# Kernel tuning notes

Hardware: AMD Instinct MI355X
Metric: run time of the kernel (lower is better)

## Reference

```python
import jax, jax.numpy as jnp
import numpy as np

B, T, D, H = 8, 2048, 2048, 128  # batch, seq_len, d_model, head_size
NEG = -1e9


def setup_inputs() -> dict:
    key = jax.random.key(0)
    k0, k1, k2, k3 = jax.random.split(key, 4)
    x = jax.random.normal(k0, (B, T, D), dtype=jnp.float32)
    s = 1.0 / np.sqrt(D)
    Wq = jax.random.normal(k1, (D, H), dtype=jnp.float32) * s
    Wk = jax.random.normal(k2, (D, H), dtype=jnp.float32) * s
    Wv = jax.random.normal(k3, (D, H), dtype=jnp.float32) * s
    return {"x": x, "Wq": Wq, "Wk": Wk, "Wv": Wv}


def reference(x, Wq, Wk, Wv):
    # projections: [B,T,H]
    q = jnp.einsum('btd,dh->bth', x, Wq)
    k = jnp.einsum('btd,dh->bth', x, Wk)
    v = jnp.einsum('btd,dh->bth', x, Wv)
    # NOTE: module multiplies by sqrt(head_size) (faithful to source)
    wei = jnp.einsum('bqh,bkh->bqk', q, k) * jnp.sqrt(jnp.float32(H))
    causal = jnp.tril(jnp.ones((T, T), dtype=bool))
    wei = jnp.where(causal, wei, jnp.float32(NEG))
    wei = jax.nn.softmax(wei, axis=-1)
    # dropout is identity (deterministic=True / rate=0)
    out = jnp.einsum('bqk,bkh->bqh', wei, v)
    return out
```

## Files before the change

kernel.cpp:

```cpp
#include <hip/hip_runtime.h>
#include <math.h>

#define B_ 8
#define T_ 2048
#define D_ 2048
#define H_ 128
#define M_ (B_ * T_)

typedef __bf16 bf16x8 __attribute__((ext_vector_type(8)));
typedef __bf16 bf16x4 __attribute__((ext_vector_type(4)));
typedef float f32x4 __attribute__((ext_vector_type(4)));

#define MFMA(a, b, c) __builtin_amdgcn_mfma_f32_16x16x32_bf16(a, b, c, 0, 0, 0)

#define QH_OFF 0
#define QL_OFF (1 * 2097152)
#define KH_OFF (2 * 2097152)
#define KL_OFF (3 * 2097152)
#define VT_OFF (4 * 2097152)
#define WTH_OFF (5 * 2097152)
#define WTL_OFF (WTH_OFF + 786432)

__global__ __launch_bounds__(256) void prep_kernel(
    const float* __restrict__ Wq, const float* __restrict__ Wk,
    const float* __restrict__ Wv, __bf16* __restrict__ wpk_hi,
    __bf16* __restrict__ wpk_lo) {
  const int z = blockIdx.y;
  const int k0 = blockIdx.x * 64;
  const float* W = z == 0 ? Wq : z == 1 ? Wk : Wv;
  __shared__ float tile[64][132];
  const int t = threadIdx.x;
#pragma unroll
  for (int it = 0; it < 8; ++it) {
    int f4 = it * 256 + t;
    int row = f4 >> 5, c = (f4 & 31) << 2;
    *(float4*)&tile[row][c] = *(const float4*)&W[(size_t)(k0 + row) * H_ + c];
  }
  __syncthreads();
  int n = t >> 1, kh = (t & 1) << 5;
  __bf16 h[32], l[32];
#pragma unroll
  for (int kk = 0; kk < 32; ++kk) {
    float x = tile[kh + kk][n];
    __bf16 hi = (__bf16)x;
    h[kk] = hi;
    l[kk] = (__bf16)(x - (float)hi);
  }
  const int nf = z * H_ + n;
  const int g = nf >> 4, l15 = nf & 15;
  const int s = (k0 + kh) >> 5;
#pragma unroll
  for (int c = 0; c < 4; ++c) {
    size_t dst = ((size_t)(g * 64 + s) * 64 + c * 16 + l15) * 8;
    *(bf16x8*)&wpk_hi[dst] = *(bf16x8*)&h[c * 8];
    *(bf16x8*)&wpk_lo[dst] = *(bf16x8*)&l[c * 8];
  }
}

#define XSTR 72

#define PROJ_STEP(KS, CH, CL, NH, NL)                                      \
  {                                                                        \
    __syncthreads();                                                       \
    {                                                                      \
      __bf16 h0 = (__bf16)xr.x, h1 = (__bf16)xr.y, h2 = (__bf16)xr.z,      \
             h3 = (__bf16)xr.w;                                            \
      bf16x4 hv = {h0, h1, h2, h3};                                        \
      bf16x4 lv = {(__bf16)(xr.x - (float)h0), (__bf16)(xr.y - (float)h1), \
                   (__bf16)(xr.z - (float)h2), (__bf16)(xr.w - (float)h3)};\
      *(bf16x4*)&Xs[xm * XSTR + xk] = hv;                                  \
      *(bf16x4*)&Xs[xm * XSTR + 32 + xk] = lv;                             \
    }                                                                      \
    if ((KS) < 63) {                                                       \
      const int ko = ((KS) + 1) << 5;                                      \
      xr = *(const float4*)(xgp + ko);                                     \
      _Pragma("unroll") for (int nt = 0; nt < 3; ++nt) {                   \
        NH[nt] = *(const bf16x8*)(wph[nt] + ((KS) + 1) * 512);             \
        NL[nt] = *(const bf16x8*)(wpl[nt] + ((KS) + 1) * 512);             \
      }                                                                    \
    }                                                                      \
    __syncthreads();                                                       \
    bf16x8 ah[2], al[2];                                                   \
    _Pragma("unroll") for (int mg = 0; mg < 2; ++mg) {                     \
      ah[mg] = *(bf16x8*)&Xs[(wr * 32 + mg * 16 + l15) * XSTR + q8];       \
      al[mg] = *(bf16x8*)&Xs[(wr * 32 + mg * 16 + l15) * XSTR + 32 + q8];  \
    }                                                                      \
    _Pragma("unroll") for (int nt = 0; nt < 3; ++nt) {                     \
      _Pragma("unroll") for (int mg = 0; mg < 2; ++mg) {                   \
        acc[mg][nt] = MFMA(ah[mg], CH[nt], acc[mg][nt]);                   \
        acc[mg][nt] = MFMA(al[mg], CH[nt], acc[mg][nt]);                   \
        acc[mg][nt] = MFMA(ah[mg], CL[nt], acc[mg][nt]);                   \
      }                                                                    \
    }                                                                      \
  }

__global__ __launch_bounds__(512, 4) void proj_kernel(
    const float* __restrict__ X, const __bf16* __restrict__ wpk_hi,
    const __bf16* __restrict__ wpk_lo, __bf16* __restrict__ qh,
    __bf16* __restrict__ ql, __bf16* __restrict__ kh,
    __bf16* __restrict__ kl, __bf16* __restrict__ vt) {
  __shared__ __align__(16) __bf16 Xs[64 * XSTR];
  const int t = threadIdx.x;
  const int wv = t >> 6, lane = t & 63;
  const int l15 = lane & 15, quad = lane >> 4, q8 = quad * 8;
  const int bi = blockIdx.x;
  const int m0 = (bi >> 1) * 64;
  const int nbase = (bi & 1) * 192;
  const int wr = wv >> 2, wc = wv & 3;
  const int xm = t >> 3, xk = (t & 7) << 2;
  const float* xgp = X + (size_t)(m0 + xm) * D_ + xk;
  const __bf16* wph[3];
  const __bf16* wpl[3];
#pragma unroll
  for (int nt = 0; nt < 3; ++nt) {
    int g = (nbase >> 4) + wc * 3 + nt;
    size_t off = (size_t)g * 32768 + (size_t)lane * 8;
    wph[nt] = wpk_hi + off;
    wpl[nt] = wpk_lo + off;
  }
  f32x4 acc[2][3] = {};
  float4 xr = *(const float4*)xgp;
  bf16x8 wha[3], wla[3], whb[3], wlb[3];
#pragma unroll
  for (int nt = 0; nt < 3; ++nt) {
    wha[nt] = *(const bf16x8*)(wph[nt]);
    wla[nt] = *(const bf16x8*)(wpl[nt]);
  }
  for (int ks2 = 0; ks2 < 64; ks2 += 2) {
    PROJ_STEP(ks2, wha, wla, whb, wlb);
    PROJ_STEP(ks2 + 1, whb, wlb, wha, wla);
  }
#pragma unroll
  for (int nt = 0; nt < 3; ++nt) {
    int ncb = nbase + wc * 48 + nt * 16;
    int z = ncb >> 7;
    int h = (ncb & 127) + l15;
#pragma unroll
    for (int mg = 0; mg < 2; ++mg) {
      int r0 = m0 + wr * 32 + mg * 16 + quad * 4;
      if (z == 2) {
        int b = m0 >> 11;
        int tt0 = (m0 & 2047) + wr * 32 + mg * 16 + quad * 4;
        bf16x4 pv = {(__bf16)acc[mg][nt][0], (__bf16)acc[mg][nt][1],
                     (__bf16)acc[mg][nt][2], (__bf16)acc[mg][nt][3]};
        *(bf16x4*)&vt[(size_t)(b * H_ + h) * T_ + tt0] = pv;
      } else {
        __bf16* dh = z == 0 ? qh : kh;
        __bf16* dl = z == 0 ? ql : kl;
#pragma unroll
        for (int reg = 0; reg < 4; ++reg) {
          float v = acc[mg][nt][reg];
          __bf16 hi = (__bf16)v;
          dh[(size_t)(r0 + reg) * H_ + h] = hi;
          dl[(size_t)(r0 + reg) * H_ + h] = (__bf16)(v - (float)hi);
        }
      }
    }
  }
}

__global__ __launch_bounds__(512, 2) void attn_kernel(
    const __bf16* __restrict__ qh, const __bf16* __restrict__ qlo,
    const __bf16* __restrict__ kh, const __bf16* __restrict__ klo,
    const __bf16* __restrict__ vt, float* __restrict__ out) {
  const int t = threadIdx.x;
  const int wv = t >> 6, st = wv >> 2, cw = wv & 3;
  const int lane = t & 63, l15 = lane & 15, quad = lane >> 4;
  const int j = blockIdx.x, b = j & 7, pi = j >> 3;
  const int qlidx = (st == 0) ? pi : 63 - pi;
  const int t0 = qlidx * 32;
  const int nkt = (qlidx >> 1) + 1;
  __shared__ __align__(16) __bf16 Pbuf[8][32 * 72];
  __shared__ __align__(16) float Obuf[2][32 * 132];
  __shared__ float mlb[2][4][32], llb[2][4][32];
  const size_t qrow0 = (size_t)b * T_ + t0;
  bf16x8 qfh[2][4], qfl[2][4];
#pragma unroll
  for (int mg = 0; mg < 2; ++mg)
#pragma unroll
    for (int ds = 0; ds < 4; ++ds) {
      size_t off = (qrow0 + mg * 16 + l15) * H_ + ds * 32 + quad * 8;
      qfh[mg][ds] = *(const bf16x8*)(qh + off);
      qfl[mg][ds] = *(const bf16x8*)(qlo + off);
    }
  f32x4 O[2][8] = {};
  float ms[2][4], ls[2][4];
#pragma unroll
  for (int mg = 0; mg < 2; ++mg)
#pragma unroll
    for (int reg = 0; reg < 4; ++reg) {
      ms[mg][reg] = -INFINITY;
      ls[mg][reg] = 0.f;
    }
  const __bf16* vtb = vt + (size_t)b * H_ * T_;
  const float scale = 11.313708498984761f;
  for (int kt_i = cw; kt_i < nkt; kt_i += 4) {
    const int kt = kt_i * 64;
    f32x4 S[2][4] = {};
#pragma unroll
    for (int ds = 0; ds < 4; ++ds)
#pragma unroll
      for (int ct = 0; ct < 4; ++ct) {
        size_t koff =
            ((size_t)b * T_ + kt + ct * 16 + l15) * H_ + ds * 32 + quad * 8;
        bf16x8 bh = *(const bf16x8*)(kh + koff);
        bf16x8 bl = *(const bf16x8*)(klo + koff);
#pragma unroll
        for (int mg = 0; mg < 2; ++mg) {
          S[mg][ct] = MFMA(qfh[mg][ds], bh, S[mg][ct]);
          S[mg][ct] = MFMA(qfl[mg][ds], bh, S[mg][ct]);
          S[mg][ct] = MFMA(qfh[mg][ds], bl, S[mg][ct]);
        }
      }
    const bool diag = (kt_i == nkt - 1);
#pragma unroll
    for (int mg = 0; mg < 2; ++mg)
#pragma unroll
      for (int ct = 0; ct < 4; ++ct)
#pragma unroll
        for (int reg = 0; reg < 4; ++reg) {
          float s = S[mg][ct][reg] * scale;
          if (diag && (kt + ct * 16 + l15 > t0 + mg * 16 + quad * 4 + reg))
            s = -1e30f;
          S[mg][ct][reg] = s;
        }
    float al_[2][4];
#pragma unroll
    for (int mg = 0; mg < 2; ++mg)
#pragma unroll
      for (int reg = 0; reg < 4; ++reg) {
        float r = fmaxf(fmaxf(S[mg][0][reg], S[mg][1][reg]),
                        fmaxf(S[mg][2][reg], S[mg][3][reg]));
        r = fmaxf(r, __shfl_xor(r, 1));
        r = fmaxf(r, __shfl_xor(r, 2));
        r = fmaxf(r, __shfl_xor(r, 4));
        r = fmaxf(r, __shfl_xor(r, 8));
        float mn = fmaxf(ms[mg][reg], r);
        float a = __expf(ms[mg][reg] - mn);
        ms[mg][reg] = mn;
        float ps = 0.f;
#pragma unroll
        for (int ct = 0; ct < 4; ++ct) {
          float p = __expf(S[mg][ct][reg] - mn);
          S[mg][ct][reg] = p;
          ps += p;
        }
        ps += __shfl_xor(ps, 1);
        ps += __shfl_xor(ps, 2);
        ps += __shfl_xor(ps, 4);
        ps += __shfl_xor(ps, 8);
        ls[mg][reg] = ls[mg][reg] * a + ps;
        al_[mg][reg] = a;
      }
#pragma unroll
    for (int mg = 0; mg < 2; ++mg)
#pragma unroll
      for (int ht = 0; ht < 8; ++ht)
#pragma unroll
        for (int reg = 0; reg < 4; ++reg) O[mg][ht][reg] *= al_[mg][reg];
#pragma unroll
    for (int mg = 0; mg < 2; ++mg)
#pragma unroll
      for (int ct = 0; ct < 4; ++ct)
#pragma unroll
        for (int reg = 0; reg < 4; ++reg)
          Pbuf[wv][(mg * 16 + quad * 4 + reg) * 72 + ct * 16 + l15] =
              (__bf16)S[mg][ct][reg];
#pragma unroll
    for (int ks = 0; ks < 2; ++ks) {
      bf16x8 pf0 = *(bf16x8*)&Pbuf[wv][(l15)*72 + ks * 32 + quad * 8];
      bf16x8 pf1 = *(bf16x8*)&Pbuf[wv][(16 + l15) * 72 + ks * 32 + quad * 8];
#pragma unroll
      for (int ht = 0; ht < 8; ++ht) {
        bf16x8 vf = *(const bf16x8*)&vtb[(size_t)(ht * 16 + l15) * T_ + kt +
                                         ks * 32 + quad * 8];
        O[0][ht] = MFMA(pf0, vf, O[0][ht]);
        O[1][ht] = MFMA(pf1, vf, O[1][ht]);
      }
    }
  }
  if (l15 == 0) {
#pragma unroll
    for (int mg = 0; mg < 2; ++mg)
#pragma unroll
      for (int reg = 0; reg < 4; ++reg) {
        mlb[st][cw][mg * 16 + quad * 4 + reg] = ms[mg][reg];
        llb[st][cw][mg * 16 + quad * 4 + reg] = ls[mg][reg];
      }
  }
  for (int i = t; i < 2 * 32 * 132; i += 512) ((float*)Obuf)[i] = 0.f;
  __syncthreads();
  float aw[2][4];
#pragma unroll
  for (int mg = 0; mg < 2; ++mg)
#pragma unroll
    for (int reg = 0; reg < 4; ++reg) {
      int row = mg * 16 + quad * 4 + reg;
      float M = fmaxf(fmaxf(mlb[st][0][row], mlb[st][1][row]),
                      fmaxf(mlb[st][2][row], mlb[st][3][row]));
      float L = 0.f;
#pragma unroll
      for (int w = 0; w < 4; ++w)
        L += llb[st][w][row] * __expf(mlb[st][w][row] - M);
      aw[mg][reg] = __expf(ms[mg][reg] - M) / L;
    }
#pragma unroll
  for (int mg = 0; mg < 2; ++mg)
#pragma unroll
    for (int ht = 0; ht < 8; ++ht)
#pragma unroll
      for (int reg = 0; reg < 4; ++reg)
        atomicAdd(&Obuf[st][(mg * 16 + quad * 4 + reg) * 132 + ht * 16 + l15],
                  O[mg][ht][reg] * aw[mg][reg]);
  __syncthreads();
  {
    const int stw = t >> 8, tt = t & 255;
    const int qlw = (stw == 0) ? pi : 63 - pi;
    const size_t obase = ((size_t)b * T_ + qlw * 32) * H_;
#pragma unroll
    for (int i = 0; i < 4; ++i) {
      int f4 = i * 256 + tt;
      int row = f4 >> 5, c = (f4 & 31) << 2;
      *(float4*)&out[obase + (size_t)row * H_ + c] =
          *(float4*)&Obuf[stw][row * 132 + c];
    }
  }
}

extern "C" void kernel_launch(void* const* d_in, const int* in_sizes, int n_in,
                              void* d_out, int out_size, void* d_ws, size_t ws_size,
                              hipStream_t stream) {
  const float* x = (const float*)d_in[0];
  const float* Wq = (const float*)d_in[1];
  const float* Wk = (const float*)d_in[2];
  const float* Wv = (const float*)d_in[3];
  __bf16* ws = (__bf16*)d_ws;
  float* out = (float*)d_out;
  prep_kernel<<<dim3(32, 3), 256, 0, stream>>>(Wq, Wk, Wv, ws + WTH_OFF,
                                               ws + WTL_OFF);
  proj_kernel<<<512, 512, 0, stream>>>(x, ws + WTH_OFF, ws + WTL_OFF,
                                       ws + QH_OFF, ws + QL_OFF, ws + KH_OFF,
                                       ws + KL_OFF, ws + VT_OFF);
  attn_kernel<<<256, 512, 0, stream>>>(ws + QH_OFF, ws + QL_OFF, ws + KH_OFF,
                                       ws + KL_OFF, ws + VT_OFF, out);
}
```

Before: 397.8 us.

## Stage projection weights through LDS and prefetch two K-steps ahead

The prep kernel now writes the split hi/lo bf16 weights in a plain transposed [N][D] layout instead of an MFMA-fragment-packed layout. The projection kernel cooperatively loads each 32-wide K slice of the weights into LDS and reads MFMA B fragments from there, so each weight element is fetched from global memory once per block rather than once per wave row. Global prefetch now runs two K-steps ahead using double register sets. In exchange it adds about 28KB of LDS traffic and extra LDS reads per step, which may reduce occupancy or cause bank conflicts.

```diff
diff --git a/kernel.cpp b/kernel.cpp
--- a/kernel.cpp
+++ b/kernel.cpp
@@ -23,8 +23,8 @@
 
 __global__ __launch_bounds__(256) void prep_kernel(
     const float* __restrict__ Wq, const float* __restrict__ Wk,
-    const float* __restrict__ Wv, __bf16* __restrict__ wpk_hi,
-    __bf16* __restrict__ wpk_lo) {
+    const float* __restrict__ Wv, __bf16* __restrict__ wt_hi,
+    __bf16* __restrict__ wt_lo) {
   const int z = blockIdx.y;
   const int k0 = blockIdx.x * 64;
   const float* W = z == 0 ? Wq : z == 1 ? Wk : Wv;
@@ -46,59 +46,78 @@
     h[kk] = hi;
     l[kk] = (__bf16)(x - (float)hi);
   }
-  const int nf = z * H_ + n;
-  const int g = nf >> 4, l15 = nf & 15;
-  const int s = (k0 + kh) >> 5;
+  size_t base = (size_t)(z * H_ + n) * D_ + k0 + kh;
 #pragma unroll
   for (int c = 0; c < 4; ++c) {
-    size_t dst = ((size_t)(g * 64 + s) * 64 + c * 16 + l15) * 8;
-    *(bf16x8*)&wpk_hi[dst] = *(bf16x8*)&h[c * 8];
-    *(bf16x8*)&wpk_lo[dst] = *(bf16x8*)&l[c * 8];
+    *(bf16x8*)&wt_hi[base + c * 8] = *(bf16x8*)&h[c * 8];
+    *(bf16x8*)&wt_lo[base + c * 8] = *(bf16x8*)&l[c * 8];
   }
 }
 
+#define WSTR 36
 #define XSTR 72
 
-#define PROJ_STEP(KS, CH, CL, NH, NL)                                      \
+#define PSTEP(KS, XR, WRG)                                                 \
   {                                                                        \
-    __syncthreads();                                                       \
+    __syncthreads();                 \
     {                                                                      \
-      __bf16 h0 = (__bf16)xr.x, h1 = (__bf16)xr.y, h2 = (__bf16)xr.z,      \
-             h3 = (__bf16)xr.w;                                            \
+      __bf16 h0 = (__bf16)XR.x, h1 = (__bf16)XR.y, h2 = (__bf16)XR.z,      \
+             h3 = (__bf16)XR.w;                                            \
       bf16x4 hv = {h0, h1, h2, h3};                                        \
-      bf16x4 lv = {(__bf16)(xr.x - (float)h0), (__bf16)(xr.y - (float)h1), \
-                   (__bf16)(xr.z - (float)h2), (__bf16)(xr.w - (float)h3)};\
+      bf16x4 lv = {(__bf16)(XR.x - (float)h0), (__bf16)(XR.y - (float)h1), \
+                   (__bf16)(XR.z - (float)h2), (__bf16)(XR.w - (float)h3)};\
       *(bf16x4*)&Xs[xm * XSTR + xk] = hv;                                  \
       *(bf16x4*)&Xs[xm * XSTR + 32 + xk] = lv;                             \
     }                                                                      \
-    if ((KS) < 63) {                                                       \
-      const int ko = ((KS) + 1) << 5;                                      \
-      xr = *(const float4*)(xgp + ko);                                     \
-      _Pragma("unroll") for (int nt = 0; nt < 3; ++nt) {                   \
-        NH[nt] = *(const bf16x8*)(wph[nt] + ((KS) + 1) * 512);             \
-        NL[nt] = *(const bf16x8*)(wpl[nt] + ((KS) + 1) * 512);             \
+    _Pragma("unroll") for (int p = 0; p < 3; ++p) {                        \
+      bf16x4 a, b;                                                         \
+      _Pragma("unroll") for (int jj = 0; jj < 4; ++jj) {                   \
+        a[jj] = WRG[p][jj];                                                \
+        b[jj] = WRG[p][jj + 4];                                            \
       }                                                                    \
-    }                                                                      \
-    __syncthreads();                                                       \
+      *(bf16x4*)(wdst[p]) = a;                                             \
+      *(bf16x4*)(wdst[p] + 4) = b;                                         \
+    }                                                                      \
+    if ((KS) < 62) {     \
+      const int ko = ((KS) + 2) << 5;                                      \
+      XR = *(const float4*)(xgp + ko);                                     \
+      _Pragma("unroll") for (int p = 0; p < 3; ++p)                        \
+        WRG[p] = *(const bf16x8*)(wsrc[p] + ko);                           \
+    }                                                                      \
+    __syncthreads();                              \
     bf16x8 ah[2], al[2];                                                   \
     _Pragma("unroll") for (int mg = 0; mg < 2; ++mg) {                     \
       ah[mg] = *(bf16x8*)&Xs[(wr * 32 + mg * 16 + l15) * XSTR + q8];       \
       al[mg] = *(bf16x8*)&Xs[(wr * 32 + mg * 16 + l15) * XSTR + 32 + q8];  \
     }                                                                      \
     _Pragma("unroll") for (int nt = 0; nt < 3; ++nt) {                     \
+      const int n = wc * 48 + nt * 16 + l15;                               \
+      bf16x4 b0 = *(bf16x4*)&Wh[n * WSTR + q8];                            \
+      bf16x4 b1 = *(bf16x4*)&Wh[n * WSTR + q8 + 4];                        \
+      bf16x4 b2 = *(bf16x4*)&Wl[n * WSTR + q8];                            \
+      bf16x4 b3 = *(bf16x4*)&Wl[n * WSTR + q8 + 4];                        \
+      bf16x8 bh, bl;                                                       \
+      _Pragma("unroll") for (int jj = 0; jj < 4; ++jj) {                   \
+        bh[jj] = b0[jj];                                                   \
+        bh[jj + 4] = b1[jj];                                               \
+        bl[jj] = b2[jj];                                                   \
+        bl[jj + 4] = b3[jj];                                               \
+      }                                                                    \
       _Pragma("unroll") for (int mg = 0; mg < 2; ++mg) {                   \
-        acc[mg][nt] = MFMA(ah[mg], CH[nt], acc[mg][nt]);                   \
-        acc[mg][nt] = MFMA(al[mg], CH[nt], acc[mg][nt]);                   \
-        acc[mg][nt] = MFMA(ah[mg], CL[nt], acc[mg][nt]);                   \
+        acc[mg][nt] = MFMA(ah[mg], bh, acc[mg][nt]);                       \
+        acc[mg][nt] = MFMA(al[mg], bh, acc[mg][nt]);                       \
+        acc[mg][nt] = MFMA(ah[mg], bl, acc[mg][nt]);                       \
       }                                                                    \
     }                                                                      \
   }
 
 __global__ __launch_bounds__(512, 4) void proj_kernel(
-    const float* __restrict__ X, const __bf16* __restrict__ wpk_hi,
-    const __bf16* __restrict__ wpk_lo, __bf16* __restrict__ qh,
+    const float* __restrict__ X, const __bf16* __restrict__ wt_hi,
+    const __bf16* __restrict__ wt_lo, __bf16* __restrict__ qh,
     __bf16* __restrict__ ql, __bf16* __restrict__ kh,
     __bf16* __restrict__ kl, __bf16* __restrict__ vt) {
+  __shared__ __align__(16) __bf16 Wh[192 * WSTR];
+  __shared__ __align__(16) __bf16 Wl[192 * WSTR];
   __shared__ __align__(16) __bf16 Xs[64 * XSTR];
   const int t = threadIdx.x;
   const int wv = t >> 6, lane = t & 63;
@@ -109,26 +128,29 @@
   const int wr = wv >> 2, wc = wv & 3;
   const int xm = t >> 3, xk = (t & 7) << 2;
   const float* xgp = X + (size_t)(m0 + xm) * D_ + xk;
-  const __bf16* wph[3];
-  const __bf16* wpl[3];
-#pragma unroll
-  for (int nt = 0; nt < 3; ++nt) {
-    int g = (nbase >> 4) + wc * 3 + nt;
-    size_t off = (size_t)g * 32768 + (size_t)lane * 8;
-    wph[nt] = wpk_hi + off;
-    wpl[nt] = wpk_lo + off;
+  const __bf16* wsrc[3];
+  __bf16* wdst[3];
+#pragma unroll
+  for (int p = 0; p < 3; ++p) {
+    int c = t + (p << 9);
+    int sel = c >= 768;
+    int cr = sel ? c - 768 : c;
+    int r = cr >> 2, o = (c & 3) << 3;
+    wsrc[p] = (sel ? wt_lo : wt_hi) + (size_t)(nbase + r) * D_ + o;
+    wdst[p] = (sel ? Wl : Wh) + r * WSTR + o;
   }
   f32x4 acc[2][3] = {};
-  float4 xr = *(const float4*)xgp;
-  bf16x8 wha[3], wla[3], whb[3], wlb[3];
-#pragma unroll
-  for (int nt = 0; nt < 3; ++nt) {
-    wha[nt] = *(const bf16x8*)(wph[nt]);
-    wla[nt] = *(const bf16x8*)(wpl[nt]);
+  float4 xrA = *(const float4*)xgp;
+  float4 xrB = *(const float4*)(xgp + 32);
+  bf16x8 wrA[3], wrB[3];
+#pragma unroll
+  for (int p = 0; p < 3; ++p) {
+    wrA[p] = *(const bf16x8*)(wsrc[p]);
+    wrB[p] = *(const bf16x8*)(wsrc[p] + 32);
   }
   for (int ks2 = 0; ks2 < 64; ks2 += 2) {
-    PROJ_STEP(ks2, wha, wla, whb, wlb);
-    PROJ_STEP(ks2 + 1, whb, wlb, wha, wla);
+    PSTEP(ks2, xrA, wrA);
+    PSTEP(ks2 + 1, xrB, wrB);
   }
 #pragma unroll
   for (int nt = 0; nt < 3; ++nt) {
```

After: 384.9 us. 1.03x faster.

## Stage projection weights through LDS via async global_load_lds with double buffering

Applied to the files above, without the earlier changes.

Weight fragments in the projection kernel are now loaded asynchronously straight into LDS with global_load_lds into a double-buffered tile. Each weight fragment is loaded once per block instead of once per column-group wave. The X tile is also double-buffered, with one float4 prefetched two steps ahead. This cuts the two barriers per K-step to one with explicit waitcnt and sched barriers, so loads overlap MFMA work. In exchange it uses more LDS (about 66KB per block), which may limit occupancy under launch_bounds(512,4), and the manual vmcnt accounting is fragile.

```diff
diff --git a/kernel.cpp b/kernel.cpp
--- a/kernel.cpp
+++ b/kernel.cpp
@@ -20,6 +20,11 @@
 #define VT_OFF (4 * 2097152)
 #define WTH_OFF (5 * 2097152)
 #define WTL_OFF (WTH_OFF + 786432)
+
+#define GL_LDS16(gp, lp)                                      \
+  __builtin_amdgcn_global_load_lds(                           \
+      (const __attribute__((address_space(1))) void*)(gp),    \
+      (__attribute__((address_space(3))) void*)(lp), 16, 0, 0)
 
 __global__ __launch_bounds__(256) void prep_kernel(
     const float* __restrict__ Wq, const float* __restrict__ Wk,
@@ -59,39 +64,50 @@
 
 #define XSTR 72
 
-#define PROJ_STEP(KS, CH, CL, NH, NL)                                      \
-  {                                                                        \
-    __syncthreads();                                                       \
-    {                                                                      \
-      __bf16 h0 = (__bf16)xr.x, h1 = (__bf16)xr.y, h2 = (__bf16)xr.z,      \
-             h3 = (__bf16)xr.w;                                            \
-      bf16x4 hv = {h0, h1, h2, h3};                                        \
-      bf16x4 lv = {(__bf16)(xr.x - (float)h0), (__bf16)(xr.y - (float)h1), \
-                   (__bf16)(xr.z - (float)h2), (__bf16)(xr.w - (float)h3)};\
-      *(bf16x4*)&Xs[xm * XSTR + xk] = hv;                                  \
-      *(bf16x4*)&Xs[xm * XSTR + 32 + xk] = lv;                             \
-    }                                                                      \
-    if ((KS) < 63) {                                                       \
-      const int ko = ((KS) + 1) << 5;                                      \
-      xr = *(const float4*)(xgp + ko);                                     \
-      _Pragma("unroll") for (int nt = 0; nt < 3; ++nt) {                   \
-        NH[nt] = *(const bf16x8*)(wph[nt] + ((KS) + 1) * 512);             \
-        NL[nt] = *(const bf16x8*)(wpl[nt] + ((KS) + 1) * 512);             \
-      }                                                                    \
-    }                                                                      \
-    __syncthreads();                                                       \
-    bf16x8 ah[2], al[2];                                                   \
-    _Pragma("unroll") for (int mg = 0; mg < 2; ++mg) {                     \
-      ah[mg] = *(bf16x8*)&Xs[(wr * 32 + mg * 16 + l15) * XSTR + q8];       \
-      al[mg] = *(bf16x8*)&Xs[(wr * 32 + mg * 16 + l15) * XSTR + 32 + q8];  \
-    }                                                                      \
-    _Pragma("unroll") for (int nt = 0; nt < 3; ++nt) {                     \
-      _Pragma("unroll") for (int mg = 0; mg < 2; ++mg) {                   \
-        acc[mg][nt] = MFMA(ah[mg], CH[nt], acc[mg][nt]);                   \
-        acc[mg][nt] = MFMA(al[mg], CH[nt], acc[mg][nt]);                   \
-        acc[mg][nt] = MFMA(ah[mg], CL[nt], acc[mg][nt]);                   \
-      }                                                                    \
-    }                                                                      \
+#define XCONV(RW, NB)                                                       \
+  {                                                                         \
+    __bf16 h0 = (__bf16)RW.x, h1 = (__bf16)RW.y, h2 = (__bf16)RW.z,         \
+           h3 = (__bf16)RW.w;                                               \
+    bf16x4 hv = {h0, h1, h2, h3};                                           \
+    bf16x4 lv = {(__bf16)(RW.x - (float)h0), (__bf16)(RW.y - (float)h1),    \
+                 (__bf16)(RW.z - (float)h2), (__bf16)(RW.w - (float)h3)};   \
+    *(bf16x4*)&Xs[NB][xm * XSTR + xk] = hv;                                 \
+    *(bf16x4*)&Xs[NB][xm * XSTR + 32 + xk] = lv;                            \
+  }
+
+#define COMPUTE(CUR)                                                        \
+  {                                                                         \
+    bf16x8 ah[2], al[2];                                                    \
+    _Pragma("unroll") for (int mg = 0; mg < 2; ++mg) {                      \
+      ah[mg] = *(bf16x8*)&Xs[CUR][(wr * 32 + mg * 16 + l15) * XSTR + q8];   \
+      al[mg] =                                                              \
+          *(bf16x8*)&Xs[CUR][(wr * 32 + mg * 16 + l15) * XSTR + 32 + q8];   \
+    }                                                                       \
+    _Pragma("unroll") for (int nt = 0; nt < 3; ++nt) {                      \
+      const int g = wc * 3 + nt;                                            \
+      bf16x8 bh = *(bf16x8*)&Wf[CUR][g * 512 + lane * 8];                   \
+      bf16x8 bl = *(bf16x8*)&Wf[CUR][6144 + g * 512 + lane * 8];            \
+      _Pragma("unroll") for (int mg = 0; mg < 2; ++mg) {                    \
+        acc[mg][nt] = MFMA(ah[mg], bh, acc[mg][nt]);                        \
+        acc[mg][nt] = MFMA(al[mg], bh, acc[mg][nt]);                        \
+        acc[mg][nt] = MFMA(ah[mg], bl, acc[mg][nt]);                        \
+      }                                                                     \
+    }                                                                       \
+  }
+
+#define PSTEP(KS, RW, RL)                                                   \
+  {                                                                         \
+    const int nb_ = ((KS)&1) ^ 1;                                           \
+    _Pragma("unroll") for (int i = 0; i < 3; ++i)                           \
+        GL_LDS16(gsrc[i] + ((KS) + 1) * 512, ldst0[i] + nb_ * 12288);       \
+    __builtin_amdgcn_sched_barrier(0);        \
+    RL = *(const float4*)(xgp + ((KS) + 2) * 32);                           \
+    XCONV(RW, nb_);                                                         \
+    COMPUTE((KS)&1);                                                        \
+    asm volatile("s_waitcnt vmcnt(1) lgkmcnt(0)" ::: "memory");             \
+    __builtin_amdgcn_sched_barrier(0);                                      \
+    __builtin_amdgcn_s_barrier();                                           \
+    __builtin_amdgcn_sched_barrier(0);                                      \
   }
 
 __global__ __launch_bounds__(512, 4) void proj_kernel(
@@ -99,7 +115,8 @@
     const __bf16* __restrict__ wpk_lo, __bf16* __restrict__ qh,
     __bf16* __restrict__ ql, __bf16* __restrict__ kh,
     __bf16* __restrict__ kl, __bf16* __restrict__ vt) {
-  __shared__ __align__(16) __bf16 Xs[64 * XSTR];
+  __shared__ __align__(16) __bf16 Wf[2][12288];
+  __shared__ __align__(16) __bf16 Xs[2][64 * XSTR];
   const int t = threadIdx.x;
   const int wv = t >> 6, lane = t & 63;
   const int l15 = lane & 15, quad = lane >> 4, q8 = quad * 8;
@@ -109,27 +126,46 @@
   const int wr = wv >> 2, wc = wv & 3;
   const int xm = t >> 3, xk = (t & 7) << 2;
   const float* xgp = X + (size_t)(m0 + xm) * D_ + xk;
-  const __bf16* wph[3];
-  const __bf16* wpl[3];
-#pragma unroll
-  for (int nt = 0; nt < 3; ++nt) {
-    int g = (nbase >> 4) + wc * 3 + nt;
-    size_t off = (size_t)g * 32768 + (size_t)lane * 8;
-    wph[nt] = wpk_hi + off;
-    wpl[nt] = wpk_lo + off;
+  const __bf16* gsrc[3];
+  __bf16* ldst0[3];
+#pragma unroll
+  for (int i = 0; i < 3; ++i) {
+    int f = wv * 3 + i;
+    int sel = f >= 12;
+    int gl = f - sel * 12;
+    int gg = (nbase >> 4) + gl;
+    gsrc[i] = (sel ? wpk_lo : wpk_hi) + (size_t)gg * 32768 + (size_t)lane * 8;
+    ldst0[i] = &Wf[0][sel * 6144 + gl * 512];
   }
   f32x4 acc[2][3] = {};
-  float4 xr = *(const float4*)xgp;
-  bf16x8 wha[3], wla[3], whb[3], wlb[3];
-#pragma unroll
-  for (int nt = 0; nt < 3; ++nt) {
-    wha[nt] = *(const bf16x8*)(wph[nt]);
-    wla[nt] = *(const bf16x8*)(wpl[nt]);
-  }
-  for (int ks2 = 0; ks2 < 64; ks2 += 2) {
-    PROJ_STEP(ks2, wha, wla, whb, wlb);
-    PROJ_STEP(ks2 + 1, whb, wlb, wha, wla);
-  }
+  {
+    float4 x0 = *(const float4*)xgp;
+#pragma unroll
+    for (int i = 0; i < 3; ++i) GL_LDS16(gsrc[i], ldst0[i]);
+    XCONV(x0, 0);
+  }
+  float4 xA = *(const float4*)(xgp + 32);
+  float4 xB;
+  asm volatile("s_waitcnt vmcnt(0) lgkmcnt(0)" ::: "memory");
+  __builtin_amdgcn_sched_barrier(0);
+  __builtin_amdgcn_s_barrier();
+  __builtin_amdgcn_sched_barrier(0);
+  for (int ks2 = 0; ks2 < 62; ks2 += 2) {
+    PSTEP(ks2, xA, xB);
+    PSTEP(ks2 + 1, xB, xA);
+  }
+  {
+#pragma unroll
+    for (int i = 0; i < 3; ++i)
+      GL_LDS16(gsrc[i] + 63 * 512, ldst0[i] + 12288);
+    XCONV(xA, 1);
+    COMPUTE(0);
+    asm volatile("s_waitcnt vmcnt(0) lgkmcnt(0)" ::: "memory");
+    __builtin_amdgcn_sched_barrier(0);
+    __builtin_amdgcn_s_barrier();
+    __builtin_amdgcn_sched_barrier(0);
+  }
+  COMPUTE(1);
 #pragma unroll
   for (int nt = 0; nt < 3; ++nt) {
     int ncb = nbase + wc * 48 + nt * 16;
```

Measured after the change: 362.0 us. 9.0% less time.
